# Optimization experiments

Hardware: AMD Instinct MI355X
Metric: run time of the kernel (lower is better)

Reference implementation:

```python
import jax, jax.numpy as jnp
import numpy as np

N_ENTITY = 30000
N_MOVIE = 6000
D = 384            # entity_hidden_size = hidden_size // 2
H = 768            # hidden_size
HT = 768           # token_hidden_size
N_LAYER = 12
N_BLOCK = 2
N_HEAD = 12
HEAD_DIM = H // N_HEAD
NUM_REL = 12
NUM_BASES = 8
E_KG = 200000
E_C = 200000
E_S = 80000
B = 16
LE = 48
LT = 256


def setup_inputs() -> dict:
    key = jax.random.key(0)
    ks = iter(jax.random.split(key, 48))
    nk = lambda: next(ks)
    rn = lambda shape, s=0.02: jax.random.normal(nk(), shape, dtype=jnp.float32) * s
    ri = lambda shape, m: jax.random.randint(nk(), shape, 0, m)
    return {
        'node_embeds': rn((N_ENTITY, D), 0.05),
        'rgcn_bases': rn((NUM_BASES, D, D)),
        'rgcn_comp': rn((NUM_REL, NUM_BASES), 0.3),
        'rgcn_root': rn((D, D)),
        'rgcn_bias': rn((D,), 0.01),
        'ep1_w1': rn((D, D // 2)), 'ep1_b1': rn((D // 2,), 0.01),
        'ep1_w2': rn((D // 2, D)), 'ep1_b2': rn((D,), 0.01),
        'ep2_w': rn((D, H)), 'ep2_b': rn((H,), 0.01),
        'tp1_w1': rn((HT, HT // 2)), 'tp1_b1': rn((HT // 2,), 0.01),
        'tp1_w2': rn((HT // 2, HT)), 'tp1_b2': rn((HT,), 0.01),
        'tp2_w': rn((HT, H)), 'tp2_b': rn((H,), 0.01),
        'ca_w': rn((H, H)),
        'pp1_w1': rn((H, H // 2)), 'pp1_b1': rn((H // 2,), 0.01),
        'pp1_w2': rn((H // 2, H)), 'pp1_b2': rn((H,), 0.01),
        'pp2_w': rn((H, N_LAYER * N_BLOCK * H)), 'pp2_b': rn((N_LAYER * N_BLOCK * H,), 0.01),
        'token_embeds': jax.random.normal(nk(), (B, LT, HT), dtype=jnp.float32),
        'edge_index': ri((2, E_KG), N_ENTITY),
        'edge_type': ri((E_KG,), NUM_REL),
        'edge_index_c': ri((2, E_C), N_ENTITY),
        'edge_index_t_s': ri((2, E_S), N_MOVIE),
        'edge_index_i_s': ri((2, E_S), N_MOVIE),
        'movie_to_entity': ri((N_MOVIE,), N_ENTITY),
        'entity_ids': ri((B, LE), N_ENTITY),
    }


def _mlp(x, w1, b1, w2, b2):
    return jax.nn.relu(x @ w1 + b1) @ w2 + b2


def _gcn(x, edge_index):
    # CustomGCNConv: add self loops, symmetric deg^{-1/2} norm, scatter-add
    n = x.shape[0]
    loop = jnp.arange(n)
    src = jnp.concatenate([edge_index[0], loop])
    dst = jnp.concatenate([edge_index[1], loop])
    deg = jax.ops.segment_sum(jnp.ones_like(dst, dtype=x.dtype), dst, num_segments=n)
    dis = deg ** -0.5  # deg >= 1 due to self loops
    norm = dis[src] * dis[dst]
    return jax.ops.segment_sum(norm[:, None] * x[src], dst, num_segments=n)


def _rgcn(x, edge_index, edge_type, bases, comp, root, bias):
    # PyG RGCNConv with basis decomposition, mean aggregation per relation
    n = x.shape[0]
    src, dst = edge_index[0], edge_index[1]
    W = jnp.einsum('rb,bio->rio', comp, bases)  # [R, D, D]
    out = x @ root + bias
    for r in range(NUM_REL):
        mask = (edge_type == r).astype(x.dtype)
        cnt = jax.ops.segment_sum(mask, dst, num_segments=n)
        norm = mask / jnp.maximum(cnt[dst], 1.0)
        h = x @ W[r]
        out = out + jax.ops.segment_sum(norm[:, None] * h[src], dst, num_segments=n)
    return out


def reference(node_embeds, rgcn_bases, rgcn_comp, rgcn_root, rgcn_bias,
              ep1_w1, ep1_b1, ep1_w2, ep1_b2, ep2_w, ep2_b,
              tp1_w1, tp1_b1, tp1_w2, tp1_b2, tp2_w, tp2_b,
              ca_w, pp1_w1, pp1_b1, pp1_w2, pp1_b2, pp2_w, pp2_b,
              token_embeds, edge_index, edge_type, edge_index_c,
              edge_index_t_s, edge_index_i_s, movie_to_entity, entity_ids):
    # ---- get_entity_embeds ----
    ent0 = _rgcn(node_embeds, edge_index, edge_type, rgcn_bases, rgcn_comp, rgcn_root, rgcn_bias) + node_embeds
    nf = ent0[movie_to_entity]  # sorted_indices == idx_to_id_tensor (keys are range(n_movie))
    ts1 = _gcn(nf, edge_index_t_s)
    ts2 = _gcn(ts1, edge_index_t_s)  # ts3 computed in original but unused -> skipped
    mt = (ts1 + ts2) * 0.5
    is1 = _gcn(nf, edge_index_i_s)
    is2 = _gcn(is1, edge_index_i_s)
    mi = (is1 + is2) * 0.5
    mm = (mt + mi) * 0.5
    c1 = _gcn(ent0, edge_index_c)
    c2 = _gcn(c1, edge_index_c)
    c3 = _gcn(c2, edge_index_c)
    ent = (c1 + c2 + c3 + ent0) * 0.25
    ent = ent.at[movie_to_entity].add(mm)  # index_add_
    ent = _mlp(ent, ep1_w1, ep1_b1, ep1_w2, ep1_b2) + ent
    ent = ent @ ep2_w + ep2_b  # [N_ENTITY, H]
    # ---- forward ----
    eemb = ent[entity_ids]  # [B, LE, H]
    tok = _mlp(token_embeds, tp1_w1, tp1_b1, tp1_w2, tp1_b2) + token_embeds
    tok = tok @ tp2_w + tp2_b  # [B, LT, H]
    attn = jnp.einsum('bth,beh->bte', tok @ ca_w, eemb) / H
    w = jax.nn.softmax(attn, axis=2)  # output_entity=False branch
    prompt = jnp.einsum('bte,beh->bth', w, eemb) + tok
    prompt = _mlp(prompt, pp1_w1, pp1_b1, pp1_w2, pp1_b2) + prompt
    prompt = prompt @ pp2_w + pp2_b  # [B, LT, N_LAYER*N_BLOCK*H]
    prompt = prompt.reshape(B, LT, N_LAYER, N_BLOCK, N_HEAD, HEAD_DIM)
    return prompt.transpose(2, 3, 0, 4, 1, 5)  # [n_layer, n_block, B, n_head, LT, head_dim]
```

## Files before the change

### kernel.cpp

```cpp
#include <hip/hip_runtime.h>
#include <hip/hip_bf16.h>
#include <cstdint>
#include <cstddef>


namespace {

constexpr int NE   = 30000;
constexpr int NM   = 6000;
constexpr int Dm   = 384;
constexpr int Hm   = 768;
constexpr int EKG  = 200000;
constexpr int EC   = 200000;
constexpr int ES   = 80000;
constexpr int Bc   = 16;
constexpr int LE   = 48;
constexpr int NTOK = 4096;
constexpr int NO   = 18432;

constexpr size_t NBf = (size_t)NE * Dm;
constexpr size_t MBF = (size_t)NM * Dm;

constexpr size_t P_XB    = 0;
constexpr size_t P_WCT   = 5760000;
constexpr size_t P_CNT   = 6644736;
constexpr size_t P_ENT0  = 7004736;
constexpr size_t P_HH    = 18524736;
constexpr size_t P_DIS   = 53084736;
constexpr size_t P_E0B   = 0;
constexpr size_t P_C1B   = 2880000;
constexpr size_t P_C2B   = 5760000;
constexpr size_t P_NFB   = 8640000;
constexpr size_t P_T1B   = 9800000;
constexpr size_t P_G1    = 11000000;
constexpr size_t P_ACC   = 41564736;
constexpr size_t P_ENTB  = 55600000;
constexpr size_t P_HIDB  = 0;
constexpr size_t P_ENT2B = 2880000;
constexpr size_t P_E768B = 8640000;
constexpr size_t P_TOKB  = 20160000;
constexpr size_t P_THIDB = 21732864;
constexpr size_t P_TOK1B = 22519296;
constexpr size_t P_TOK2B = 24092160;
constexpr size_t P_QB    = 25665024;
constexpr size_t P_EEMB  = 27237888;
constexpr size_t P_PR0   = 27532800;
constexpr size_t P_PR0B  = 30678528;
constexpr size_t P_PHIDB = 32251392;
constexpr size_t P_WT    = 74000000;
constexpr size_t S_ROOT  = 0;
constexpr size_t S_EP1A  = 147456;
constexpr size_t S_EP1B  = 221184;
constexpr size_t S_EP2   = 294912;
constexpr size_t S_TP1A  = 589824;
constexpr size_t S_TP1B  = 884736;
constexpr size_t S_TP2   = 1179648;
constexpr size_t S_CAW   = 1769472;
constexpr size_t S_PP1A  = 2359296;
constexpr size_t S_PP1B  = 2654208;

constexpr size_t WI       = 6291456 / 4;
constexpr size_t I_CNT    = WI + 0;
constexpr size_t I_PART   = WI + 30000;
constexpr size_t I_KG_RP  = WI + 30256;
constexpr size_t I_KG_CA  = WI + 60256;
constexpr size_t I_KG_SL  = WI + 90256;
constexpr size_t I_C_RP   = WI + 290256;
constexpr size_t I_C_CUR  = WI + 320256;
constexpr size_t I_C_SL   = WI + 350256;
constexpr size_t I_TS_RP  = WI + 550256;
constexpr size_t I_TS_CUR = WI + 556256;
constexpr size_t I_TS_SL  = WI + 562256;
constexpr size_t I_IS_RP  = WI + 642256;
constexpr size_t I_IS_CUR = WI + 648256;
constexpr size_t I_IS_SL  = WI + 654256;
constexpr size_t I_KG_BND = WI + 734256;
constexpr size_t I_KG_CB  = WI + 764256;
constexpr size_t WS_PP2T_BYTE = 6291456;
constexpr size_t WS_NEED      = 34603008;

inline int cdiv(long a, long b) { return (int)((a + b - 1) / b); }

}

typedef short short8v __attribute__((ext_vector_type(8)));
typedef float f32x4 __attribute__((ext_vector_type(4)));

__device__ __forceinline__ unsigned short f2bf(float f) {
  union { float f; uint32_t u; } v; v.f = f;
  uint32_t u = v.u;
  u += 0x7fffu + ((u >> 16) & 1u);
  return (unsigned short)(u >> 16);
}
__device__ __forceinline__ uint32_t pkbf(float a, float b) {
  __hip_bfloat162 h = __float22bfloat162_rn(float2{a, b});
  union { __hip_bfloat162 h; uint32_t u; } cv; cv.h = h;
  return cv.u;
}
__device__ __forceinline__ float bflo(uint32_t u) {
  union { uint32_t u; float f; } c; c.u = u << 16; return c.f;
}
__device__ __forceinline__ float bfhi(uint32_t u) {
  union { uint32_t u; float f; } c; c.u = u & 0xFFFF0000u; return c.f;
}

__device__ __forceinline__ void gl16(const void* g, void* l) {
  __builtin_amdgcn_global_load_lds(
      (const __attribute__((address_space(1))) void*)g,
      (__attribute__((address_space(3))) void*)l, 16, 0, 0);
}


__global__ void k_cvt(const float* __restrict__ x, unsigned short* __restrict__ o, size_t n2) {
  size_t i = (size_t)blockIdx.x * 256 + threadIdx.x;
  if (i >= n2) return;
  float2 v = *(const float2*)(x + 2 * i);
  *(uint32_t*)(o + 2 * i) = pkbf(v.x, v.y);
}

__global__ void k_cvt_t(const float* __restrict__ W, unsigned short* __restrict__ Wt,
                        int K, int N) {
  __shared__ float t[32][33];
  int tx = threadIdx.x & 31, ty = threadIdx.x >> 5;
  int n0 = blockIdx.x * 32, k0 = blockIdx.y * 32;
#pragma unroll
  for (int j = 0; j < 4; ++j)
    t[ty + 8 * j][tx] = W[(size_t)(k0 + ty + 8 * j) * N + n0 + tx];
  __syncthreads();
#pragma unroll
  for (int j = 0; j < 4; ++j) {
    int n = ty + 8 * j;
    Wt[(size_t)(n0 + n) * K + k0 + tx] = f2bf(t[tx][n]);
  }
}

__global__ void k_wcat(const float* __restrict__ comp, const float* __restrict__ bases,
                       unsigned short* __restrict__ Wt) {
  int idx = blockIdx.x * 256 + threadIdx.x;
  if (idx >= 12 * Dm * Dm) return;
  int i = idx % Dm;
  int o = (idx / Dm) % Dm;
  int r = idx / (Dm * Dm);
  float s = 0.f;
#pragma unroll
  for (int b = 0; b < 8; ++b)
    s += comp[r * 8 + b] * bases[(size_t)b * Dm * Dm + (size_t)i * Dm + o];
  Wt[idx] = f2bf(s);
}

__global__ void k_gather_b(const int* __restrict__ idx, const uint32_t* __restrict__ x2,
                           uint32_t* __restrict__ out2, int rows, int D2) {
  size_t i = (size_t)blockIdx.x * 256 + threadIdx.x;
  if (i >= (size_t)rows * D2) return;
  int r = (int)(i / D2);
  int c = (int)(i - (size_t)r * D2);
  out2[i] = x2[(size_t)idx[r] * D2 + c];
}

__global__ void k_scatter_movie(const int* __restrict__ mte, const float* __restrict__ g,
                                float* __restrict__ ent) {
  size_t i = (size_t)blockIdx.x * 256 + threadIdx.x;
  if (i >= MBF) return;
  int m = (int)(i / Dm);
  int d = (int)(i - (size_t)m * Dm);
  atomicAdd(&ent[(size_t)mte[m] * Dm + d], 0.25f * g[i]);
}


__global__ void k_hist(const int* __restrict__ dst, int* __restrict__ cnt, int E) {
  int e = blockIdx.x * 256 + threadIdx.x;
  if (e < E) atomicAdd(&cnt[dst[e]], 1);
}

__global__ void k_hist_lt(const int* __restrict__ dst, const int* __restrict__ typ,
                          int* __restrict__ cnt, int E) {
  int e = blockIdx.x * 256 + threadIdx.x;
  if (e < E && typ[e] < 6) atomicAdd(&cnt[dst[e]], 1);
}

__global__ void k_add_i(const int* __restrict__ a, const int* __restrict__ b,
                        int* __restrict__ o, int n) {
  int i = blockIdx.x * 256 + threadIdx.x;
  if (i < n) o[i] = a[i] + b[i];
}

__global__ void k_scan_blk(const int* __restrict__ in, int* __restrict__ out,
                           int* __restrict__ part, int n) {
  __shared__ int s[256];
  int t = threadIdx.x;
  int g = blockIdx.x * 256 + t;
  int v = (g < n) ? in[g] : 0;
  s[t] = v;
  __syncthreads();
  for (int off = 1; off < 256; off <<= 1) {
    int add = (t >= off) ? s[t - off] : 0;
    __syncthreads();
    s[t] += add;
    __syncthreads();
  }
  if (g < n) out[g] = s[t] - v;
  if (t == 255) part[blockIdx.x] = s[255];
}

__global__ void k_scan_top(int* __restrict__ part, int nb) {
  __shared__ int s[256];
  int t = threadIdx.x;
  int v = (t < nb) ? part[t] : 0;
  s[t] = v;
  __syncthreads();
  for (int off = 1; off < 256; off <<= 1) {
    int add = (t >= off) ? s[t - off] : 0;
    __syncthreads();
    s[t] += add;
    __syncthreads();
  }
  if (t < nb) part[t] = s[t] - v;
}

__global__ void k_scan_add(int* __restrict__ out, const int* __restrict__ part, int n) {
  int g = blockIdx.x * 256 + threadIdx.x;
  if (g < n) out[g] += part[blockIdx.x];
}

__global__ void k_fill(const int* __restrict__ src, const int* __restrict__ dst,
                       int* __restrict__ cur, int* __restrict__ slots, int E) {
  int e = blockIdx.x * 256 + threadIdx.x;
  if (e >= E) return;
  int d = dst[e];
  int pos = atomicAdd(&cur[d], 1);
  slots[pos] = src[e];
}

__global__ void k_fill_split(const int* __restrict__ src, const int* __restrict__ dst,
                             const int* __restrict__ typ, int* __restrict__ cur_a,
                             int* __restrict__ cur_b, int* __restrict__ slots, int E) {
  int e = blockIdx.x * 256 + threadIdx.x;
  if (e >= E) return;
  int d = dst[e];
  int* c = (typ[e] < 6) ? cur_a : cur_b;
  int pos = atomicAdd(&c[d], 1);
  slots[pos] = src[e] | (typ[e] << 16);
}

__global__ void k_dis_rp(const int* __restrict__ rp, float* __restrict__ dis, int n, int E) {
  int v = blockIdx.x * 256 + threadIdx.x;
  if (v >= n) return;
  int e0 = rp[v], e1 = (v + 1 < n) ? rp[v + 1] : E;
  dis[v] = rsqrtf((float)(e1 - e0) + 1.0f);
}

__global__ void k_count_type(const int* __restrict__ dst, const int* __restrict__ typ,
                             float* __restrict__ cnt, int E) {
  int i = blockIdx.x * 256 + threadIdx.x;
  if (i < E) atomicAdd(&cnt[(size_t)typ[i] * NE + dst[i]], 1.0f);
}

__global__ void k_rcp(float* __restrict__ c, size_t n) {
  size_t i = (size_t)blockIdx.x * 256 + threadIdx.x;
  if (i < n) { float v = c[i]; c[i] = (v > 0.f) ? 1.0f / v : 0.f; }
}

template <int OUTM, int ACCM>
__global__ void k_gcn_gb(const unsigned short* __restrict__ x,
                         const float* __restrict__ dis,
                         const int* __restrict__ rp, const int* __restrict__ slots,
                         unsigned short* __restrict__ outb, float* __restrict__ acc,
                         int n, int E, float sc) {
  int v = (int)((blockIdx.x * (size_t)blockDim.x + threadIdx.x) >> 6);
  int lane = threadIdx.x & 63;
  if (v >= n) return;
  float dv = dis[v];
  const uint32_t* xr = (const uint32_t*)(x + (size_t)v * Dm);
  float xv[6];
#pragma unroll
  for (int i = 0; i < 3; ++i) {
    uint32_t u = xr[lane + 64 * i];
    xv[2 * i] = bflo(u); xv[2 * i + 1] = bfhi(u);
  }
  float a[6];
#pragma unroll
  for (int i = 0; i < 6; ++i) a[i] = dv * xv[i];
  int e0 = rp[v], e1 = (v + 1 < n) ? rp[v + 1] : E;
  int e = e0;
  for (; e + 2 <= e1; e += 2) {
    int s0 = slots[e], s1 = slots[e + 1];
    float c0 = dis[s0], c1 = dis[s1];
    const uint32_t* x0 = (const uint32_t*)(x + (size_t)s0 * Dm);
    const uint32_t* x1 = (const uint32_t*)(x + (size_t)s1 * Dm);
    uint32_t u0[3], u1[3];
#pragma unroll
    for (int i = 0; i < 3; ++i) { u0[i] = x0[lane + 64 * i]; u1[i] = x1[lane + 64 * i]; }
#pragma unroll
    for (int i = 0; i < 3; ++i) {
      a[2 * i]     = fmaf(c0, bflo(u0[i]), a[2 * i]);
      a[2 * i + 1] = fmaf(c0, bfhi(u0[i]), a[2 * i + 1]);
      a[2 * i]     = fmaf(c1, bflo(u1[i]), a[2 * i]);
      a[2 * i + 1] = fmaf(c1, bfhi(u1[i]), a[2 * i + 1]);
    }
  }
  if (e < e1) {
    int s0 = slots[e];
    float c0 = dis[s0];
    const uint32_t* x0 = (const uint32_t*)(x + (size_t)s0 * Dm);
#pragma unroll
    for (int i = 0; i < 3; ++i) {
      uint32_t u = x0[lane + 64 * i];
      a[2 * i]     = fmaf(c0, bflo(u), a[2 * i]);
      a[2 * i + 1] = fmaf(c0, bfhi(u), a[2 * i + 1]);
    }
  }
#pragma unroll
  for (int i = 0; i < 6; ++i) a[i] *= dv;
  if (OUTM == 1) {
    uint32_t* ob = (uint32_t*)(outb + (size_t)v * Dm);
#pragma unroll
    for (int i = 0; i < 3; ++i) ob[lane + 64 * i] = pkbf(a[2 * i], a[2 * i + 1]);
  }
  float* ar = acc + (size_t)v * Dm;
  float nw[6];
#pragma unroll
  for (int i = 0; i < 3; ++i) {
    int cidx = 2 * (lane + 64 * i);
    if (ACCM == 1) {
      float2 old = *(const float2*)(ar + cidx);
      nw[2 * i] = old.x + sc * a[2 * i];
      nw[2 * i + 1] = old.y + sc * a[2 * i + 1];
    } else if (ACCM == 2) {
      nw[2 * i] = sc * (xv[2 * i] + a[2 * i]);
      nw[2 * i + 1] = sc * (xv[2 * i + 1] + a[2 * i + 1]);
    } else {
      nw[2 * i] = sc * a[2 * i];
      nw[2 * i + 1] = sc * a[2 * i + 1];
    }
    *(float2*)(ar + cidx) = float2{nw[2 * i], nw[2 * i + 1]};
  }
  if (OUTM == 2) {
    uint32_t* ob = (uint32_t*)(outb + (size_t)v * Dm);
#pragma unroll
    for (int i = 0; i < 3; ++i) ob[lane + 64 * i] = pkbf(nw[2 * i], nw[2 * i + 1]);
  }
}

template <bool FIRST, bool EMITB>
__global__ void k_rgcn_g(const unsigned short* __restrict__ hh, const float* __restrict__ rcp,
                         const int* __restrict__ rp, const int* __restrict__ bnd,
                         const int* __restrict__ slots, float* __restrict__ ent0,
                         unsigned short* __restrict__ outb, int E) {
  int v = (int)((blockIdx.x * (size_t)blockDim.x + threadIdx.x) >> 6);
  int lane = threadIdx.x & 63;
  if (v >= NE) return;
  const int rbase = FIRST ? 0 : 6;
  int e0, e1;
  if (FIRST) { e0 = rp[v]; e1 = bnd[v]; }
  else       { e0 = bnd[v]; e1 = (v + 1 < NE) ? rp[v + 1] : E; }
  float* er = ent0 + (size_t)v * Dm;
  float2 a[3];
#pragma unroll
  for (int i = 0; i < 3; ++i) a[i] = *(const float2*)(er + 2 * lane + 128 * i);
  int e = e0;
  for (; e + 2 <= e1; e += 2) {
    int p0 = slots[e], p1 = slots[e + 1];
    int r0 = (p0 >> 16) - rbase, s0 = p0 & 0xFFFF;
    int r1 = (p1 >> 16) - rbase, s1 = p1 & 0xFFFF;
    float nm0 = rcp[(size_t)(r0 + rbase) * NE + v];
    float nm1 = rcp[(size_t)(r1 + rbase) * NE + v];
    const uint32_t* h0 = (const uint32_t*)(hh + (size_t)s0 * 2304 + (size_t)r0 * 384);
    const uint32_t* h1 = (const uint32_t*)(hh + (size_t)s1 * 2304 + (size_t)r1 * 384);
    uint32_t u0[3], u1[3];
#pragma unroll
    for (int i = 0; i < 3; ++i) { u0[i] = h0[lane + 64 * i]; u1[i] = h1[lane + 64 * i]; }
#pragma unroll
    for (int i = 0; i < 3; ++i) {
      a[i].x = fmaf(nm0, bflo(u0[i]), a[i].x);
      a[i].y = fmaf(nm0, bfhi(u0[i]), a[i].y);
      a[i].x = fmaf(nm1, bflo(u1[i]), a[i].x);
      a[i].y = fmaf(nm1, bfhi(u1[i]), a[i].y);
    }
  }
  if (e < e1) {
    int p0 = slots[e];
    int r0 = (p0 >> 16) - rbase, s0 = p0 & 0xFFFF;
    float nm0 = rcp[(size_t)(r0 + rbase) * NE + v];
    const uint32_t* h0 = (const uint32_t*)(hh + (size_t)s0 * 2304 + (size_t)r0 * 384);
#pragma unroll
    for (int i = 0; i < 3; ++i) {
      uint32_t u = h0[lane + 64 * i];
      a[i].x = fmaf(nm0, bflo(u), a[i].x);
      a[i].y = fmaf(nm0, bfhi(u), a[i].y);
    }
  }
#pragma unroll
  for (int i = 0; i < 3; ++i) *(float2*)(er + 2 * lane + 128 * i) = a[i];
  if (EMITB) {
    uint32_t* ob = (uint32_t*)(outb + (size_t)v * Dm);
#pragma unroll
    for (int i = 0; i < 3; ++i) ob[lane + 64 * i] = pkbf(a[i].x, a[i].y);
  }
}

template <bool RELU, bool RES, int OUT>
__global__ __launch_bounds__(256) void mgemm_bf(
    const unsigned short* __restrict__ A, const unsigned short* __restrict__ Wt,
    const float* __restrict__ bias, const float* __restrict__ Rp,
    void* __restrict__ Cv, int M, int N, int K) {
  __shared__ __align__(16) unsigned short As[128 * 64];
  __shared__ __align__(16) unsigned short Bs[128 * 64];
  const int tid = threadIdx.x;
  const int lane = tid & 63;
  const int w = tid >> 6;
  const int bm = blockIdx.x * 128, bn = blockIdx.y * 128;
  const int wr = (w >> 1) * 64, wc = (w & 1) * 64;
  const int lrow = lane & 15, lq = lane >> 4;
  f32x4 acc[4][4] = {};
  const int prow_l = lane >> 3;
  const int pslot = lane & 7;

  for (int k0 = 0; k0 < K; k0 += 64) {
    __syncthreads();
#pragma unroll
    for (int j = 0; j < 4; ++j) {
      int seg = j * 4 + w;
      int prow = seg * 8 + prow_l;
      int aslot = pslot ^ (prow & 7);
      int arow = min(bm + prow, M - 1);
      gl16(A + (size_t)arow * K + k0 + aslot * 8, &As[seg * 512 + lane * 8]);
    }
#pragma unroll
    for (int j = 0; j < 4; ++j) {
      int seg = j * 4 + w;
      int prow = seg * 8 + prow_l;
      int bslot = pslot ^ (prow & 7);
      int brow = min(bn + prow, N - 1);
      gl16(Wt + (size_t)brow * K + k0 + bslot * 8, &Bs[seg * 512 + lane * 8]);
    }
    __syncthreads();
#pragma unroll
    for (int ks = 0; ks < 2; ++ks) {
      short8v af[4], bf[4];
      const int slot = ks * 4 + lq;
#pragma unroll
      for (int mr = 0; mr < 4; ++mr) {
        int r = wr + mr * 16 + lrow;
        af[mr] = *(const short8v*)&As[r * 64 + ((slot ^ (r & 7)) << 3)];
      }
#pragma unroll
      for (int nc = 0; nc < 4; ++nc) {
        int r = wc + nc * 16 + lrow;
        bf[nc] = *(const short8v*)&Bs[r * 64 + ((slot ^ (r & 7)) << 3)];
      }
#pragma unroll
      for (int mr = 0; mr < 4; ++mr)
#pragma unroll
        for (int nc = 0; nc < 4; ++nc)
          acc[mr][nc] = __builtin_amdgcn_mfma_f32_16x16x32_bf16(
              af[mr], bf[nc], acc[mr][nc], 0, 0, 0);
    }
  }
#pragma unroll
  for (int mr = 0; mr < 4; ++mr) {
#pragma unroll
    for (int e = 0; e < 4; ++e) {
      int r = bm + wr + mr * 16 + lq * 4 + e;
      if (r >= M) continue;
#pragma unroll
      for (int nc = 0; nc < 4; ++nc) {
        int c = bn + wc + nc * 16 + lrow;
        if (c >= N) continue;
        float v = acc[mr][nc][e];
        if (bias) v += bias[c];
        if (RES) v += Rp[(size_t)r * N + c];
        if (RELU) v = fmaxf(v, 0.f);
        if (OUT == 0) {
          ((float*)Cv)[(size_t)r * N + c] = v;
        } else if (OUT == 1) {
          ((unsigned short*)Cv)[(size_t)r * N + c] = f2bf(v);
        } else {
          int b = r >> 8, t = r & 255;
          int l = c / 1536, rem = c - l * 1536;
          int blk = rem / 768, rem2 = rem - blk * 768;
          int hh = rem2 >> 6, dd = rem2 & 63;
          size_t oi = (((((size_t)l * 2 + blk) * 16 + b) * 12 + hh) * 256 + t) * 64 + dd;
          ((float*)Cv)[oi] = v;
        }
      }
    }
  }
}

__global__ __launch_bounds__(256) void mgemm_fin(
    const unsigned short* __restrict__ A, const float* __restrict__ W,
    const float* __restrict__ bias, float* __restrict__ O, int M, int N, int K) {
  __shared__ __align__(16) unsigned short As[128 * 64];
  __shared__ __align__(16) unsigned short Bs[128 * 64];
  const int tid = threadIdx.x;
  const int lane = tid & 63;
  const int w = tid >> 6;
  const int bm = blockIdx.x * 128, bn = blockIdx.y * 128;
  const int wr = (w >> 1) * 64, wc = (w & 1) * 64;
  const int lrow = lane & 15, lq = lane >> 4;
  f32x4 acc[4][4] = {};
  const int prow_l = lane >> 3;
  const int pslot = lane & 7;
  const int n_loc = tid & 127;
  const int kh = (tid >> 7) * 32;

  for (int k0 = 0; k0 < K; k0 += 64) {
    __syncthreads();
#pragma unroll
    for (int j = 0; j < 4; ++j) {
      int seg = j * 4 + w;
      int prow = seg * 8 + prow_l;
      int aslot = pslot ^ (prow & 7);
      gl16(A + (size_t)(bm + prow) * K + k0 + aslot * 8, &As[seg * 512 + lane * 8]);
    }
    float wv[32];
    const float* wp = W + (size_t)(k0 + kh) * N + bn + n_loc;
#pragma unroll
    for (int j = 0; j < 32; ++j) wv[j] = wp[(size_t)j * N];
#pragma unroll
    for (int c = 0; c < 4; ++c) {
      uint32_t u0 = pkbf(wv[8 * c + 0], wv[8 * c + 1]);
      uint32_t u1 = pkbf(wv[8 * c + 2], wv[8 * c + 3]);
      uint32_t u2 = pkbf(wv[8 * c + 4], wv[8 * c + 5]);
      uint32_t u3 = pkbf(wv[8 * c + 6], wv[8 * c + 7]);
      int s = (kh >> 3) + c;
      *(uint4*)&Bs[n_loc * 64 + ((s ^ (n_loc & 7)) << 3)] = uint4{u0, u1, u2, u3};
    }
    __syncthreads();
#pragma unroll
    for (int ks = 0; ks < 2; ++ks) {
      short8v af[4], bf[4];
      const int slot = ks * 4 + lq;
#pragma unroll
      for (int mr = 0; mr < 4; ++mr) {
        int r = wr + mr * 16 + lrow;
        af[mr] = *(const short8v*)&As[r * 64 + ((slot ^ (r & 7)) << 3)];
      }
#pragma unroll
      for (int nc = 0; nc < 4; ++nc) {
        int r = wc + nc * 16 + lrow;
        bf[nc] = *(const short8v*)&Bs[r * 64 + ((slot ^ (r & 7)) << 3)];
      }
#pragma unroll
      for (int mr = 0; mr < 4; ++mr)
#pragma unroll
        for (int nc = 0; nc < 4; ++nc)
          acc[mr][nc] = __builtin_amdgcn_mfma_f32_16x16x32_bf16(
              af[mr], bf[nc], acc[mr][nc], 0, 0, 0);
    }
  }
#pragma unroll
  for (int mr = 0; mr < 4; ++mr) {
#pragma unroll
    for (int e = 0; e < 4; ++e) {
      int r = bm + wr + mr * 16 + lq * 4 + e;
      int b = r >> 8, t = r & 255;
#pragma unroll
      for (int nc = 0; nc < 4; ++nc) {
        int c = bn + wc + nc * 16 + lrow;
        float v = acc[mr][nc][e] + bias[c];
        int l = c / 1536, rem = c - l * 1536;
        int blk = rem / 768, rem2 = rem - blk * 768;
        int hh = rem2 >> 6, dd = rem2 & 63;
        size_t oi = (((((size_t)l * 2 + blk) * 16 + b) * 12 + hh) * 256 + t) * 64 + dd;
        O[oi] = v;
      }
    }
  }
}

__global__ __launch_bounds__(256) void k_attn(
    const unsigned short* __restrict__ qb, const unsigned short* __restrict__ eb_all,
    const unsigned short* __restrict__ tokb, float* __restrict__ pr0,
    unsigned short* __restrict__ pr0b) {
  int gw = (int)((blockIdx.x * (size_t)blockDim.x + threadIdx.x) >> 6);
  int lane = threadIdx.x & 63;
  if (gw >= NTOK) return;
  int b = gw >> 8;
  const unsigned short* qr = qb + (size_t)gw * Hm;
  float2 q[6];
#pragma unroll
  for (int i = 0; i < 6; ++i) {
    uint32_t u = *(const uint32_t*)(qr + 2 * lane + 128 * i);
    q[i] = float2{bflo(u), bfhi(u)};
  }
  const unsigned short* eb = eb_all + (size_t)b * LE * Hm;
  float myA = -3.0e38f;
  for (int e = 0; e < LE; ++e) {
    const unsigned short* er = eb + (size_t)e * Hm;
    float s = 0.f;
#pragma unroll
    for (int i = 0; i < 6; ++i) {
      uint32_t u = *(const uint32_t*)(er + 2 * lane + 128 * i);
      s = fmaf(q[i].x, bflo(u), s);
      s = fmaf(q[i].y, bfhi(u), s);
    }
#pragma unroll
    for (int off = 32; off > 0; off >>= 1) s += __shfl_xor(s, off);
    if (lane == e) myA = s * (1.0f / 768.0f);
  }
  float mx = myA;
#pragma unroll
  for (int off = 32; off > 0; off >>= 1) mx = fmaxf(mx, __shfl_xor(mx, off));
  float p = (lane < LE) ? expf(myA - mx) : 0.f;
  float sum = p;
#pragma unroll
  for (int off = 32; off > 0; off >>= 1) sum += __shfl_xor(sum, off);
  float wgt = p / sum;
  const unsigned short* tr = tokb + (size_t)gw * Hm;
  float2 a[6];
#pragma unroll
  for (int i = 0; i < 6; ++i) {
    uint32_t u = *(const uint32_t*)(tr + 2 * lane + 128 * i);
    a[i] = float2{bflo(u), bfhi(u)};
  }
  for (int e = 0; e < LE; ++e) {
    float we = __shfl(wgt, e);
    const unsigned short* er = eb + (size_t)e * Hm;
#pragma unroll
    for (int i = 0; i < 6; ++i) {
      uint32_t u = *(const uint32_t*)(er + 2 * lane + 128 * i);
      a[i].x = fmaf(we, bflo(u), a[i].x);
      a[i].y = fmaf(we, bfhi(u), a[i].y);
    }
  }
  float* orow = pr0 + (size_t)gw * Hm;
  unsigned short* obrow = pr0b + (size_t)gw * Hm;
#pragma unroll
  for (int i = 0; i < 6; ++i) {
    *(float2*)(orow + 2 * lane + 128 * i) = a[i];
    *(uint32_t*)(obrow + 2 * lane + 128 * i) = pkbf(a[i].x, a[i].y);
  }
}


extern "C" void kernel_launch(void* const* d_in, const int* in_sizes, int n_in,
                              void* d_out, int out_size, void* d_ws, size_t ws_size,
                              hipStream_t stream) {
  (void)in_sizes; (void)n_in; (void)out_size;

  const float* x_node = (const float*)d_in[0];
  const float* bases  = (const float*)d_in[1];
  const float* comp   = (const float*)d_in[2];
  const float* root   = (const float*)d_in[3];
  const float* rbias  = (const float*)d_in[4];
  const float* ep1w1  = (const float*)d_in[5];
  const float* ep1b1  = (const float*)d_in[6];
  const float* ep1w2  = (const float*)d_in[7];
  const float* ep1b2  = (const float*)d_in[8];
  const float* ep2w   = (const float*)d_in[9];
  const float* ep2b   = (const float*)d_in[10];
  const float* tp1w1  = (const float*)d_in[11];
  const float* tp1b1  = (const float*)d_in[12];
  const float* tp1w2  = (const float*)d_in[13];
  const float* tp1b2  = (const float*)d_in[14];
  const float* tp2w   = (const float*)d_in[15];
  const float* tp2b   = (const float*)d_in[16];
  const float* caw    = (const float*)d_in[17];
  const float* pp1w1  = (const float*)d_in[18];
  const float* pp1b1  = (const float*)d_in[19];
  const float* pp1w2  = (const float*)d_in[20];
  const float* pp1b2  = (const float*)d_in[21];
  const float* pp2w   = (const float*)d_in[22];
  const float* pp2b   = (const float*)d_in[23];
  const float* tokens = (const float*)d_in[24];
  const int* ei_kg = (const int*)d_in[25];
  const int* etype = (const int*)d_in[26];
  const int* ei_c  = (const int*)d_in[27];
  const int* ei_ts = (const int*)d_in[28];
  const int* ei_is = (const int*)d_in[29];
  const int* mte   = (const int*)d_in[30];
  const int* eids  = (const int*)d_in[31];

  float* O = (float*)d_out;
  unsigned short* xb    = (unsigned short*)(O + P_XB);
  unsigned short* wct   = (unsigned short*)(O + P_WCT);
  float* rcpc  = O + P_CNT;
  float* ent0  = O + P_ENT0;
  unsigned short* hh    = (unsigned short*)(O + P_HH);
  float* disc  = O + P_DIS;
  float* dist  = O + P_DIS + 30000;
  float* disi  = O + P_DIS + 36000;
  unsigned short* ent0b = (unsigned short*)(O + P_E0B);
  unsigned short* c1b   = (unsigned short*)(O + P_C1B);
  unsigned short* c2b   = (unsigned short*)(O + P_C2B);
  unsigned short* nfb   = (unsigned short*)(O + P_NFB);
  unsigned short* t1b   = (unsigned short*)(O + P_T1B);
  float* g1    = O + P_G1;
  float* accb  = O + P_ACC;
  unsigned short* entb  = (unsigned short*)(O + P_ENTB);
  unsigned short* hidb  = (unsigned short*)(O + P_HIDB);
  unsigned short* ent2b = (unsigned short*)(O + P_ENT2B);
  unsigned short* e768b = (unsigned short*)(O + P_E768B);
  unsigned short* tokb  = (unsigned short*)(O + P_TOKB);
  unsigned short* thidb = (unsigned short*)(O + P_THIDB);
  unsigned short* tok1b = (unsigned short*)(O + P_TOK1B);
  unsigned short* tok2b = (unsigned short*)(O + P_TOK2B);
  unsigned short* qb    = (unsigned short*)(O + P_QB);
  unsigned short* eemb  = (unsigned short*)(O + P_EEMB);
  float* pr0   = O + P_PR0;
  unsigned short* pr0b  = (unsigned short*)(O + P_PR0B);
  unsigned short* phidb = (unsigned short*)(O + P_PHIDB);
  unsigned short* wts   = (unsigned short*)(O + P_WT);

  int* iws = (int*)d_ws;
  unsigned short* p2b = (unsigned short*)d_ws;
  unsigned short* pp2t = (unsigned short*)d_ws + WS_PP2T_BYTE / 2;
  const bool ws_ok = (ws_size >= WS_NEED);
  int* cnt_i  = iws + I_CNT;
  int* part   = iws + I_PART;
  int* kg_rp  = iws + I_KG_RP;  int* kg_ca = iws + I_KG_CA;  int* kg_sl = iws + I_KG_SL;
  int* kg_bnd = iws + I_KG_BND; int* kg_cb = iws + I_KG_CB;
  int* c_rp   = iws + I_C_RP;   int* c_cur  = iws + I_C_CUR;   int* c_sl  = iws + I_C_SL;
  int* ts_rp  = iws + I_TS_RP;  int* ts_cur = iws + I_TS_CUR;  int* ts_sl = iws + I_TS_SL;
  int* is_rp  = iws + I_IS_RP;  int* is_cur = iws + I_IS_CUR;  int* is_sl = iws + I_IS_SL;

  const int EW = 256;

  k_cvt<<<cdiv(NBf / 2, EW), EW, 0, stream>>>(x_node, xb, NBf / 2);
  k_wcat<<<cdiv(12 * Dm * Dm, EW), EW, 0, stream>>>(comp, bases, wct);
  k_cvt_t<<<dim3(Dm / 32, Dm / 32), 256, 0, stream>>>(root, wts + S_ROOT, Dm, Dm);
  k_cvt_t<<<dim3(192 / 32, Dm / 32), 256, 0, stream>>>(ep1w1, wts + S_EP1A, Dm, 192);
  k_cvt_t<<<dim3(Dm / 32, 192 / 32), 256, 0, stream>>>(ep1w2, wts + S_EP1B, 192, Dm);
  k_cvt_t<<<dim3(Hm / 32, Dm / 32), 256, 0, stream>>>(ep2w, wts + S_EP2, Dm, Hm);
  k_cvt_t<<<dim3(Dm / 32, Hm / 32), 256, 0, stream>>>(tp1w1, wts + S_TP1A, Hm, Dm);
  k_cvt_t<<<dim3(Hm / 32, Dm / 32), 256, 0, stream>>>(tp1w2, wts + S_TP1B, Dm, Hm);
  k_cvt_t<<<dim3(Hm / 32, Hm / 32), 256, 0, stream>>>(tp2w, wts + S_TP2, Hm, Hm);
  k_cvt_t<<<dim3(Hm / 32, Hm / 32), 256, 0, stream>>>(caw, wts + S_CAW, Hm, Hm);
  k_cvt_t<<<dim3(Dm / 32, Hm / 32), 256, 0, stream>>>(pp1w1, wts + S_PP1A, Hm, Dm);
  k_cvt_t<<<dim3(Hm / 32, Dm / 32), 256, 0, stream>>>(pp1w2, wts + S_PP1B, Dm, Hm);

  hipMemsetAsync(cnt_i, 0, (size_t)NE * 4, stream);
  k_hist<<<cdiv(EKG, EW), EW, 0, stream>>>(ei_kg + EKG, cnt_i, EKG);
  {
    int nb = cdiv(NE, 256);
    k_scan_blk<<<nb, 256, 0, stream>>>(cnt_i, kg_rp, part, NE);
    k_scan_top<<<1, 256, 0, stream>>>(part, nb);
    k_scan_add<<<nb, 256, 0, stream>>>(kg_rp, part, NE);
  }
  hipMemsetAsync(cnt_i, 0, (size_t)NE * 4, stream);
  k_hist_lt<<<cdiv(EKG, EW), EW, 0, stream>>>(ei_kg + EKG, etype, cnt_i, EKG);
  k_add_i<<<cdiv(NE, EW), EW, 0, stream>>>(kg_rp, cnt_i, kg_bnd, NE);
  hipMemcpyAsync(kg_ca, kg_rp, (size_t)NE * 4, hipMemcpyDeviceToDevice, stream);
  hipMemcpyAsync(kg_cb, kg_bnd, (size_t)NE * 4, hipMemcpyDeviceToDevice, stream);
  k_fill_split<<<cdiv(EKG, EW), EW, 0, stream>>>(
      ei_kg, ei_kg + EKG, etype, kg_ca, kg_cb, kg_sl, EKG);

  auto build_csr = [&](const int* ei, int n, int E, int* rp, int* cur, int* sl) {
    hipMemsetAsync(cnt_i, 0, (size_t)n * 4, stream);
    k_hist<<<cdiv(E, EW), EW, 0, stream>>>(ei + E, cnt_i, E);
    int nb = cdiv(n, 256);
    k_scan_blk<<<nb, 256, 0, stream>>>(cnt_i, rp, part, n);
    k_scan_top<<<1, 256, 0, stream>>>(part, nb);
    k_scan_add<<<nb, 256, 0, stream>>>(rp, part, n);
    hipMemcpyAsync(cur, rp, (size_t)n * 4, hipMemcpyDeviceToDevice, stream);
    k_fill<<<cdiv(E, EW), EW, 0, stream>>>(ei, ei + E, cur, sl, E);
  };
  build_csr(ei_c, NE, EC, c_rp, c_cur, c_sl);
  build_csr(ei_ts, NM, ES, ts_rp, ts_cur, ts_sl);
  build_csr(ei_is, NM, ES, is_rp, is_cur, is_sl);

  k_dis_rp<<<cdiv(NE, EW), EW, 0, stream>>>(c_rp, disc, NE, EC);
  k_dis_rp<<<cdiv(NM, EW), EW, 0, stream>>>(ts_rp, dist, NM, ES);
  k_dis_rp<<<cdiv(NM, EW), EW, 0, stream>>>(is_rp, disi, NM, ES);

  hipMemsetAsync(rcpc, 0, (size_t)12 * NE * 4, stream);
  k_count_type<<<cdiv(EKG, EW), EW, 0, stream>>>(ei_kg + EKG, etype, rcpc, EKG);
  k_rcp<<<cdiv((long)12 * NE, EW), EW, 0, stream>>>(rcpc, (size_t)12 * NE);

  mgemm_bf<false, true, 0><<<dim3(cdiv(NE, 128), cdiv(Dm, 128)), 256, 0, stream>>>(
      xb, wts + S_ROOT, rbias, x_node, ent0, NE, Dm, Dm);
  mgemm_bf<false, false, 1><<<dim3(cdiv(NE, 128), cdiv(6 * Dm, 128)), 256, 0, stream>>>(
      xb, wct, nullptr, nullptr, hh, NE, 6 * Dm, Dm);
  k_rgcn_g<true, false><<<cdiv((long)NE * 64, EW), EW, 0, stream>>>(
      hh, rcpc, kg_rp, kg_bnd, kg_sl, ent0, nullptr, EKG);
  mgemm_bf<false, false, 1><<<dim3(cdiv(NE, 128), cdiv(6 * Dm, 128)), 256, 0, stream>>>(
      xb, wct + (size_t)6 * Dm * Dm, nullptr, nullptr, hh, NE, 6 * Dm, Dm);
  k_rgcn_g<false, true><<<cdiv((long)NE * 64, EW), EW, 0, stream>>>(
      hh, rcpc, kg_rp, kg_bnd, kg_sl, ent0, ent0b, EKG);

  k_gather_b<<<cdiv((long)NM * 192, EW), EW, 0, stream>>>(
      mte, (const uint32_t*)ent0b, (uint32_t*)nfb, NM, 192);
  k_gcn_gb<1, 3><<<cdiv((long)NM * 64, EW), EW, 0, stream>>>(
      nfb, dist, ts_rp, ts_sl, t1b, g1, NM, ES, 1.0f);
  k_gcn_gb<0, 1><<<cdiv((long)NM * 64, EW), EW, 0, stream>>>(
      t1b, dist, ts_rp, ts_sl, nullptr, g1, NM, ES, 1.0f);
  k_gcn_gb<1, 1><<<cdiv((long)NM * 64, EW), EW, 0, stream>>>(
      nfb, disi, is_rp, is_sl, t1b, g1, NM, ES, 1.0f);
  k_gcn_gb<0, 1><<<cdiv((long)NM * 64, EW), EW, 0, stream>>>(
      t1b, disi, is_rp, is_sl, nullptr, g1, NM, ES, 1.0f);
  k_gcn_gb<1, 2><<<cdiv((long)NE * 64, EW), EW, 0, stream>>>(
      ent0b, disc, c_rp, c_sl, c1b, accb, NE, EC, 0.25f);
  k_gcn_gb<1, 1><<<cdiv((long)NE * 64, EW), EW, 0, stream>>>(
      c1b, disc, c_rp, c_sl, c2b, accb, NE, EC, 0.25f);
  k_scatter_movie<<<cdiv(MBF, EW), EW, 0, stream>>>(mte, g1, accb);
  k_gcn_gb<2, 1><<<cdiv((long)NE * 64, EW), EW, 0, stream>>>(
      c2b, disc, c_rp, c_sl, entb, accb, NE, EC, 0.25f);

  if (ws_ok) {
    k_cvt_t<<<dim3(NO / 32, Hm / 32), 256, 0, stream>>>(pp2w, pp2t, Hm, NO);
  }

  mgemm_bf<true, false, 1><<<dim3(cdiv(NE, 128), cdiv(192, 128)), 256, 0, stream>>>(
      entb, wts + S_EP1A, ep1b1, nullptr, hidb, NE, 192, Dm);
  mgemm_bf<false, true, 1><<<dim3(cdiv(NE, 128), cdiv(Dm, 128)), 256, 0, stream>>>(
      hidb, wts + S_EP1B, ep1b2, accb, ent2b, NE, Dm, 192);
  mgemm_bf<false, false, 1><<<dim3(cdiv(NE, 128), cdiv(Hm, 128)), 256, 0, stream>>>(
      ent2b, wts + S_EP2, ep2b, nullptr, e768b, NE, Hm, Dm);

  k_cvt<<<cdiv((long)NTOK * Hm / 2, EW), EW, 0, stream>>>(tokens, tokb, (size_t)NTOK * Hm / 2);
  mgemm_bf<true, false, 1><<<dim3(cdiv(NTOK, 128), cdiv(Dm, 128)), 256, 0, stream>>>(
      tokb, wts + S_TP1A, tp1b1, nullptr, thidb, NTOK, Dm, Hm);
  mgemm_bf<false, true, 1><<<dim3(cdiv(NTOK, 128), cdiv(Hm, 128)), 256, 0, stream>>>(
      thidb, wts + S_TP1B, tp1b2, tokens, tok1b, NTOK, Hm, Dm);
  mgemm_bf<false, false, 1><<<dim3(cdiv(NTOK, 128), cdiv(Hm, 128)), 256, 0, stream>>>(
      tok1b, wts + S_TP2, tp2b, nullptr, tok2b, NTOK, Hm, Hm);
  mgemm_bf<false, false, 1><<<dim3(cdiv(NTOK, 128), cdiv(Hm, 128)), 256, 0, stream>>>(
      tok2b, wts + S_CAW, nullptr, nullptr, qb, NTOK, Hm, Hm);

  k_gather_b<<<cdiv((long)Bc * LE * (Hm / 2), EW), EW, 0, stream>>>(
      eids, (const uint32_t*)e768b, (uint32_t*)eemb, Bc * LE, Hm / 2);
  k_attn<<<cdiv((long)NTOK * 64, 256), 256, 0, stream>>>(qb, eemb, tok2b, pr0, pr0b);

  mgemm_bf<true, false, 1><<<dim3(cdiv(NTOK, 128), cdiv(Dm, 128)), 256, 0, stream>>>(
      pr0b, wts + S_PP1A, pp1b1, nullptr, phidb, NTOK, Dm, Hm);
  mgemm_bf<false, true, 1><<<dim3(cdiv(NTOK, 128), cdiv(Hm, 128)), 256, 0, stream>>>(
      phidb, wts + S_PP1B, pp1b2, pr0, p2b, NTOK, Hm, Dm);

  if (ws_ok) {
    mgemm_bf<false, false, 2><<<dim3(NTOK / 128, NO / 128), 256, 0, stream>>>(
        p2b, pp2t, pp2b, nullptr, O, NTOK, NO, Hm);
  } else {
    mgemm_fin<<<dim3(NTOK / 128, NO / 128), 256, 0, stream>>>(
        p2b, pp2w, pp2b, O, NTOK, NO, Hm);
  }
}
```

Before: 1.638 ms.

## Reorder RGCN to aggregate-then-transform per relation and precompute output scatter offsets

```diff
diff --git a/kernel.cpp b/kernel.cpp
--- a/kernel.cpp
+++ b/kernel.cpp
@@ -63,19 +63,18 @@
 constexpr size_t I_CNT    = WI + 0;
 constexpr size_t I_PART   = WI + 30000;
 constexpr size_t I_KG_RP  = WI + 30256;
-constexpr size_t I_KG_CA  = WI + 60256;
-constexpr size_t I_KG_SL  = WI + 90256;
-constexpr size_t I_C_RP   = WI + 290256;
-constexpr size_t I_C_CUR  = WI + 320256;
-constexpr size_t I_C_SL   = WI + 350256;
-constexpr size_t I_TS_RP  = WI + 550256;
-constexpr size_t I_TS_CUR = WI + 556256;
-constexpr size_t I_TS_SL  = WI + 562256;
-constexpr size_t I_IS_RP  = WI + 642256;
-constexpr size_t I_IS_CUR = WI + 648256;
-constexpr size_t I_IS_SL  = WI + 654256;
-constexpr size_t I_KG_BND = WI + 734256;
-constexpr size_t I_KG_CB  = WI + 764256;
+constexpr size_t I_KG_SL  = WI + 60256;
+constexpr size_t I_C_RP   = WI + 260256;
+constexpr size_t I_C_CUR  = WI + 290256;
+constexpr size_t I_C_SL   = WI + 320256;
+constexpr size_t I_TS_RP  = WI + 520256;
+constexpr size_t I_TS_CUR = WI + 526256;
+constexpr size_t I_TS_SL  = WI + 532256;
+constexpr size_t I_IS_RP  = WI + 612256;
+constexpr size_t I_IS_CUR = WI + 618256;
+constexpr size_t I_IS_SL  = WI + 624256;
+constexpr size_t I_BND12  = WI + 704256;
+constexpr size_t I_CUR12  = WI + 1064256;
 constexpr size_t WS_PP2T_BYTE = 6291456;
 constexpr size_t WS_NEED      = 34603008;
 
@@ -134,18 +133,20 @@
   }
 }
 
-__global__ void k_wcat(const float* __restrict__ comp, const float* __restrict__ bases,
-                       unsigned short* __restrict__ Wt) {
+__global__ void k_wcat2(const float* __restrict__ comp, const float* __restrict__ bases,
+                        unsigned short* __restrict__ Wt) {
   int idx = blockIdx.x * 256 + threadIdx.x;
   if (idx >= 12 * Dm * Dm) return;
   int i = idx % Dm;
-  int o = (idx / Dm) % Dm;
-  int r = idx / (Dm * Dm);
+  int rr = (idx / Dm) % 6;
+  int o = (idx / (Dm * 6)) % Dm;
+  int half = idx / (Dm * 6 * Dm);
+  int r = half * 6 + rr;
   float s = 0.f;
 #pragma unroll
   for (int b = 0; b < 8; ++b)
     s += comp[r * 8 + b] * bases[(size_t)b * Dm * Dm + (size_t)i * Dm + o];
-  Wt[idx] = f2bf(s);
+  Wt[(size_t)half * 884736 + (size_t)o * 2304 + rr * 384 + i] = f2bf(s);
 }
 
 __global__ void k_gather_b(const int* __restrict__ idx, const uint32_t* __restrict__ x2,
@@ -170,18 +171,6 @@
 __global__ void k_hist(const int* __restrict__ dst, int* __restrict__ cnt, int E) {
   int e = blockIdx.x * 256 + threadIdx.x;
   if (e < E) atomicAdd(&cnt[dst[e]], 1);
-}
-
-__global__ void k_hist_lt(const int* __restrict__ dst, const int* __restrict__ typ,
-                          int* __restrict__ cnt, int E) {
-  int e = blockIdx.x * 256 + threadIdx.x;
-  if (e < E && typ[e] < 6) atomicAdd(&cnt[dst[e]], 1);
-}
-
-__global__ void k_add_i(const int* __restrict__ a, const int* __restrict__ b,
-                        int* __restrict__ o, int n) {
-  int i = blockIdx.x * 256 + threadIdx.x;
-  if (i < n) o[i] = a[i] + b[i];
 }
 
 __global__ void k_scan_blk(const int* __restrict__ in, int* __restrict__ out,
@@ -231,15 +220,25 @@
   slots[pos] = src[e];
 }
 
-__global__ void k_fill_split(const int* __restrict__ src, const int* __restrict__ dst,
-                             const int* __restrict__ typ, int* __restrict__ cur_a,
-                             int* __restrict__ cur_b, int* __restrict__ slots, int E) {
+__global__ void k_seg(const float* __restrict__ cnt, const int* __restrict__ rp,
+                      int* __restrict__ bnd12, int n) {
+  int v = blockIdx.x * 256 + threadIdx.x;
+  if (v >= n) return;
+  int base = rp[v];
+#pragma unroll
+  for (int r = 0; r < 12; ++r) {
+    bnd12[v * 12 + r] = base;
+    base += (int)cnt[(size_t)r * NE + v];
+  }
+}
+
+__global__ void k_fill_kg(const int* __restrict__ src, const int* __restrict__ dst,
+                          const int* __restrict__ typ, int* __restrict__ cur12,
+                          int* __restrict__ slots, int E) {
   int e = blockIdx.x * 256 + threadIdx.x;
   if (e >= E) return;
-  int d = dst[e];
-  int* c = (typ[e] < 6) ? cur_a : cur_b;
-  int pos = atomicAdd(&c[d], 1);
-  slots[pos] = src[e] | (typ[e] << 16);
+  int pos = atomicAdd(&cur12[dst[e] * 12 + typ[e]], 1);
+  slots[pos] = src[e];
 }
 
 __global__ void k_dis_rp(const int* __restrict__ rp, float* __restrict__ dis, int n, int E) {
@@ -258,6 +257,43 @@
 __global__ void k_rcp(float* __restrict__ c, size_t n) {
   size_t i = (size_t)blockIdx.x * 256 + threadIdx.x;
   if (i < n) { float v = c[i]; c[i] = (v > 0.f) ? 1.0f / v : 0.f; }
+}
+
+template <bool FIRST>
+__global__ void k_agg6(const unsigned short* __restrict__ xb, const float* __restrict__ rcp,
+                       const int* __restrict__ rp, const int* __restrict__ bnd12,
+                       const int* __restrict__ slots, unsigned short* __restrict__ agg,
+                       int E) {
+  int v = (int)((blockIdx.x * (size_t)blockDim.x + threadIdx.x) >> 6);
+  int lane = threadIdx.x & 63;
+  if (v >= NE) return;
+  const int rbase = FIRST ? 0 : 6;
+  float a[6][6] = {};
+#pragma unroll
+  for (int rr = 0; rr < 6; ++rr) {
+    int rg = rbase + rr;
+    int e0 = bnd12[v * 12 + rg];
+    int e1 = (rg == 11) ? ((v + 1 < NE) ? rp[v + 1] : E) : bnd12[v * 12 + rg + 1];
+    for (int e = e0; e < e1; ++e) {
+      int s = slots[e];
+      const uint32_t* xs = (const uint32_t*)(xb + (size_t)s * Dm);
+#pragma unroll
+      for (int i = 0; i < 3; ++i) {
+        uint32_t u = xs[lane + 64 * i];
+        a[rr][2 * i]     += bflo(u);
+        a[rr][2 * i + 1] += bfhi(u);
+      }
+    }
+    float nm = rcp[(size_t)rg * NE + v];
+#pragma unroll
+    for (int i = 0; i < 6; ++i) a[rr][i] *= nm;
+  }
+  uint32_t* ag = (uint32_t*)(agg + (size_t)v * 2304);
+#pragma unroll
+  for (int rr = 0; rr < 6; ++rr)
+#pragma unroll
+    for (int i = 0; i < 3; ++i)
+      ag[rr * 192 + lane + 64 * i] = pkbf(a[rr][2 * i], a[rr][2 * i + 1]);
 }
 
 template <int OUTM, int ACCM>
@@ -338,63 +374,6 @@
     uint32_t* ob = (uint32_t*)(outb + (size_t)v * Dm);
 #pragma unroll
     for (int i = 0; i < 3; ++i) ob[lane + 64 * i] = pkbf(nw[2 * i], nw[2 * i + 1]);
-  }
-}
-
-template <bool FIRST, bool EMITB>
-__global__ void k_rgcn_g(const unsigned short* __restrict__ hh, const float* __restrict__ rcp,
-                         const int* __restrict__ rp, const int* __restrict__ bnd,
-                         const int* __restrict__ slots, float* __restrict__ ent0,
-                         unsigned short* __restrict__ outb, int E) {
-  int v = (int)((blockIdx.x * (size_t)blockDim.x + threadIdx.x) >> 6);
-  int lane = threadIdx.x & 63;
-  if (v >= NE) return;
-  const int rbase = FIRST ? 0 : 6;
-  int e0, e1;
-  if (FIRST) { e0 = rp[v]; e1 = bnd[v]; }
-  else       { e0 = bnd[v]; e1 = (v + 1 < NE) ? rp[v + 1] : E; }
-  float* er = ent0 + (size_t)v * Dm;
-  float2 a[3];
-#pragma unroll
-  for (int i = 0; i < 3; ++i) a[i] = *(const float2*)(er + 2 * lane + 128 * i);
-  int e = e0;
-  for (; e + 2 <= e1; e += 2) {
-    int p0 = slots[e], p1 = slots[e + 1];
-    int r0 = (p0 >> 16) - rbase, s0 = p0 & 0xFFFF;
-    int r1 = (p1 >> 16) - rbase, s1 = p1 & 0xFFFF;
-    float nm0 = rcp[(size_t)(r0 + rbase) * NE + v];
-    float nm1 = rcp[(size_t)(r1 + rbase) * NE + v];
-    const uint32_t* h0 = (const uint32_t*)(hh + (size_t)s0 * 2304 + (size_t)r0 * 384);
-    const uint32_t* h1 = (const uint32_t*)(hh + (size_t)s1 * 2304 + (size_t)r1 * 384);
-    uint32_t u0[3], u1[3];
-#pragma unroll
-    for (int i = 0; i < 3; ++i) { u0[i] = h0[lane + 64 * i]; u1[i] = h1[lane + 64 * i]; }
-#pragma unroll
-    for (int i = 0; i < 3; ++i) {
-      a[i].x = fmaf(nm0, bflo(u0[i]), a[i].x);
-      a[i].y = fmaf(nm0, bfhi(u0[i]), a[i].y);
-      a[i].x = fmaf(nm1, bflo(u1[i]), a[i].x);
-      a[i].y = fmaf(nm1, bfhi(u1[i]), a[i].y);
-    }
-  }
-  if (e < e1) {
-    int p0 = slots[e];
-    int r0 = (p0 >> 16) - rbase, s0 = p0 & 0xFFFF;
-    float nm0 = rcp[(size_t)(r0 + rbase) * NE + v];
-    const uint32_t* h0 = (const uint32_t*)(hh + (size_t)s0 * 2304 + (size_t)r0 * 384);
-#pragma unroll
-    for (int i = 0; i < 3; ++i) {
-      uint32_t u = h0[lane + 64 * i];
-      a[i].x = fmaf(nm0, bflo(u), a[i].x);
-      a[i].y = fmaf(nm0, bfhi(u), a[i].y);
-    }
-  }
-#pragma unroll
-  for (int i = 0; i < 3; ++i) *(float2*)(er + 2 * lane + 128 * i) = a[i];
-  if (EMITB) {
-    uint32_t* ob = (uint32_t*)(outb + (size_t)v * Dm);
-#pragma unroll
-    for (int i = 0; i < 3; ++i) ob[lane + 64 * i] = pkbf(a[i].x, a[i].y);
   }
 }
 
@@ -456,12 +435,25 @@
               af[mr], bf[nc], acc[mr][nc], 0, 0, 0);
     }
   }
+  size_t colb[4];
+  if (OUT == 2) {
+#pragma unroll
+    for (int nc = 0; nc < 4; ++nc) {
+      int c = bn + wc + nc * 16 + lrow;
+      int l = c / 1536, rem = c - l * 1536;
+      int blk = rem / 768, rem2 = rem - blk * 768;
+      int h2 = rem2 >> 6, dd = rem2 & 63;
+      colb[nc] = (size_t)(l * 2 + blk) * 3145728 + (size_t)h2 * 16384 + dd;
+    }
+  }
 #pragma unroll
   for (int mr = 0; mr < 4; ++mr) {
 #pragma unroll
     for (int e = 0; e < 4; ++e) {
       int r = bm + wr + mr * 16 + lq * 4 + e;
       if (r >= M) continue;
+      size_t rowoff = 0;
+      if (OUT == 2) rowoff = (size_t)r * 64 + (size_t)(r >> 8) * 180224;
 #pragma unroll
       for (int nc = 0; nc < 4; ++nc) {
         int c = bn + wc + nc * 16 + lrow;
@@ -475,12 +467,7 @@
         } else if (OUT == 1) {
           ((unsigned short*)Cv)[(size_t)r * N + c] = f2bf(v);
         } else {
-          int b = r >> 8, t = r & 255;
-          int l = c / 1536, rem = c - l * 1536;
-          int blk = rem / 768, rem2 = rem - blk * 768;
-          int hh = rem2 >> 6, dd = rem2 & 63;
-          size_t oi = (((((size_t)l * 2 + blk) * 16 + b) * 12 + hh) * 256 + t) * 64 + dd;
-          ((float*)Cv)[oi] = v;
+          ((float*)Cv)[colb[nc] + rowoff] = v;
         }
       }
     }
@@ -674,10 +661,10 @@
 
   float* O = (float*)d_out;
   unsigned short* xb    = (unsigned short*)(O + P_XB);
-  unsigned short* wct   = (unsigned short*)(O + P_WCT);
+  unsigned short* wct2  = (unsigned short*)(O + P_WCT);
   float* rcpc  = O + P_CNT;
   float* ent0  = O + P_ENT0;
-  unsigned short* hh    = (unsigned short*)(O + P_HH);
+  unsigned short* aggb  = (unsigned short*)(O + P_HH);
   float* disc  = O + P_DIS;
   float* dist  = O + P_DIS + 30000;
   float* disi  = O + P_DIS + 36000;
@@ -709,8 +696,8 @@
   const bool ws_ok = (ws_size >= WS_NEED);
   int* cnt_i  = iws + I_CNT;
   int* part   = iws + I_PART;
-  int* kg_rp  = iws + I_KG_RP;  int* kg_ca = iws + I_KG_CA;  int* kg_sl = iws + I_KG_SL;
-  int* kg_bnd = iws + I_KG_BND; int* kg_cb = iws + I_KG_CB;
+  int* kg_rp  = iws + I_KG_RP;  int* kg_sl = iws + I_KG_SL;
+  int* bnd12  = iws + I_BND12;  int* cur12 = iws + I_CUR12;
   int* c_rp   = iws + I_C_RP;   int* c_cur  = iws + I_C_CUR;   int* c_sl  = iws + I_C_SL;
   int* ts_rp  = iws + I_TS_RP;  int* ts_cur = iws + I_TS_CUR;  int* ts_sl = iws + I_TS_SL;
   int* is_rp  = iws + I_IS_RP;  int* is_cur = iws + I_IS_CUR;  int* is_sl = iws + I_IS_SL;
@@ -718,7 +705,7 @@
   const int EW = 256;
 
   k_cvt<<<cdiv(NBf / 2, EW), EW, 0, stream>>>(x_node, xb, NBf / 2);
-  k_wcat<<<cdiv(12 * Dm * Dm, EW), EW, 0, stream>>>(comp, bases, wct);
+  k_wcat2<<<cdiv(12 * Dm * Dm, EW), EW, 0, stream>>>(comp, bases, wct2);
   k_cvt_t<<<dim3(Dm / 32, Dm / 32), 256, 0, stream>>>(root, wts + S_ROOT, Dm, Dm);
   k_cvt_t<<<dim3(192 / 32, Dm / 32), 256, 0, stream>>>(ep1w1, wts + S_EP1A, Dm, 192);
   k_cvt_t<<<dim3(Dm / 32, 192 / 32), 256, 0, stream>>>(ep1w2, wts + S_EP1B, 192, Dm);
@@ -730,6 +717,8 @@
   k_cvt_t<<<dim3(Dm / 32, Hm / 32), 256, 0, stream>>>(pp1w1, wts + S_PP1A, Hm, Dm);
   k_cvt_t<<<dim3(Hm / 32, Dm / 32), 256, 0, stream>>>(pp1w2, wts + S_PP1B, Dm, Hm);
 
+  hipMemsetAsync(rcpc, 0, (size_t)12 * NE * 4, stream);
+  k_count_type<<<cdiv(EKG, EW), EW, 0, stream>>>(ei_kg + EKG, etype, rcpc, EKG);
   hipMemsetAsync(cnt_i, 0, (size_t)NE * 4, stream);
   k_hist<<<cdiv(EKG, EW), EW, 0, stream>>>(ei_kg + EKG, cnt_i, EKG);
   {
@@ -738,13 +727,10 @@
     k_scan_top<<<1, 256, 0, stream>>>(part, nb);
     k_scan_add<<<nb, 256, 0, stream>>>(kg_rp, part, NE);
   }
-  hipMemsetAsync(cnt_i, 0, (size_t)NE * 4, stream);
-  k_hist_lt<<<cdiv(EKG, EW), EW, 0, stream>>>(ei_kg + EKG, etype, cnt_i, EKG);
-  k_add_i<<<cdiv(NE, EW), EW, 0, stream>>>(kg_rp, cnt_i, kg_bnd, NE);
-  hipMemcpyAsync(kg_ca, kg_rp, (size_t)NE * 4, hipMemcpyDeviceToDevice, stream);
-  hipMemcpyAsync(kg_cb, kg_bnd, (size_t)NE * 4, hipMemcpyDeviceToDevice, stream);
-  k_fill_split<<<cdiv(EKG, EW), EW, 0, stream>>>(
-      ei_kg, ei_kg + EKG, etype, kg_ca, kg_cb, kg_sl, EKG);
+  k_seg<<<cdiv(NE, EW), EW, 0, stream>>>(rcpc, kg_rp, bnd12, NE);
+  hipMemcpyAsync(cur12, bnd12, (size_t)NE * 12 * 4, hipMemcpyDeviceToDevice, stream);
+  k_fill_kg<<<cdiv(EKG, EW), EW, 0, stream>>>(ei_kg, ei_kg + EKG, etype, cur12, kg_sl, EKG);
+  k_rcp<<<cdiv((long)12 * NE, EW), EW, 0, stream>>>(rcpc, (size_t)12 * NE);
 
   auto build_csr = [&](const int* ei, int n, int E, int* rp, int* cur, int* sl) {
     hipMemsetAsync(cnt_i, 0, (size_t)n * 4, stream);
@@ -764,20 +750,17 @@
   k_dis_rp<<<cdiv(NM, EW), EW, 0, stream>>>(ts_rp, dist, NM, ES);
   k_dis_rp<<<cdiv(NM, EW), EW, 0, stream>>>(is_rp, disi, NM, ES);
 
-  hipMemsetAsync(rcpc, 0, (size_t)12 * NE * 4, stream);
-  k_count_type<<<cdiv(EKG, EW), EW, 0, stream>>>(ei_kg + EKG, etype, rcpc, EKG);
-  k_rcp<<<cdiv((long)12 * NE, EW), EW, 0, stream>>>(rcpc, (size_t)12 * NE);
-
   mgemm_bf<false, true, 0><<<dim3(cdiv(NE, 128), cdiv(Dm, 128)), 256, 0, stream>>>(
       xb, wts + S_ROOT, rbias, x_node, ent0, NE, Dm, Dm);
-  mgemm_bf<false, false, 1><<<dim3(cdiv(NE, 128), cdiv(6 * Dm, 128)), 256, 0, stream>>>(
-      xb, wct, nullptr, nullptr, hh, NE, 6 * Dm, Dm);
-  k_rgcn_g<true, false><<<cdiv((long)NE * 64, EW), EW, 0, stream>>>(
-      hh, rcpc, kg_rp, kg_bnd, kg_sl, ent0, nullptr, EKG);
-  mgemm_bf<false, false, 1><<<dim3(cdiv(NE, 128), cdiv(6 * Dm, 128)), 256, 0, stream>>>(
-      xb, wct + (size_t)6 * Dm * Dm, nullptr, nullptr, hh, NE, 6 * Dm, Dm);
-  k_rgcn_g<false, true><<<cdiv((long)NE * 64, EW), EW, 0, stream>>>(
-      hh, rcpc, kg_rp, kg_bnd, kg_sl, ent0, ent0b, EKG);
+  k_agg6<true><<<cdiv((long)NE * 64, EW), EW, 0, stream>>>(
+      xb, rcpc, kg_rp, bnd12, kg_sl, aggb, EKG);
+  mgemm_bf<false, true, 0><<<dim3(cdiv(NE, 128), cdiv(Dm, 128)), 256, 0, stream>>>(
+      aggb, wct2, nullptr, ent0, ent0, NE, Dm, 6 * Dm);
+  k_agg6<false><<<cdiv((long)NE * 64, EW), EW, 0, stream>>>(
+      xb, rcpc, kg_rp, bnd12, kg_sl, aggb, EKG);
+  mgemm_bf<false, true, 0><<<dim3(cdiv(NE, 128), cdiv(Dm, 128)), 256, 0, stream>>>(
+      aggb, wct2 + 884736, nullptr, ent0, ent0, NE, Dm, 6 * Dm);
+  k_cvt<<<cdiv(NBf / 2, EW), EW, 0, stream>>>(ent0, ent0b, NBf / 2);
 
   k_gather_b<<<cdiv((long)NM * 192, EW), EW, 0, stream>>>(
       mte, (const uint32_t*)ent0b, (uint32_t*)nfb, NM, 192);
```

Result: no change. 1.663 ms (+1.6%).
